# Performance work log

Hardware: AMD Instinct MI355X
Metric: run time of the kernel (lower is better)

## Reference

```python
import jax, jax.numpy as jnp
import numpy as np
import math

EMB, HEAD, B, S = 1024, 64, 4, 4096

def setup_inputs() -> dict:
    key = jax.random.key(0)
    ks = jax.random.split(key, 7)
    scale = 1.0 / math.sqrt(EMB)
    return {
        "x": jax.random.normal(ks[0], (B, S, EMB), dtype=jnp.float32),
        "Wq": jax.random.uniform(ks[1], (EMB, HEAD), jnp.float32, -scale, scale),
        "bq": jax.random.uniform(ks[2], (HEAD,), jnp.float32, -scale, scale),
        "Wk": jax.random.uniform(ks[3], (EMB, HEAD), jnp.float32, -scale, scale),
        "bk": jax.random.uniform(ks[4], (HEAD,), jnp.float32, -scale, scale),
        "Wv": jax.random.uniform(ks[5], (EMB, HEAD), jnp.float32, -scale, scale),
        "bv": jax.random.uniform(ks[6], (HEAD,), jnp.float32, -scale, scale),
    }

def reference(x, Wq, bq, Wk, bk, Wv, bv):
    # x: [B, S, E]
    q = x @ Wq + bq            # [B, S, H]
    k = x @ Wk + bk
    v = x @ Wv + bv
    scores = jnp.einsum('bqh,bkh->bqk', q, k) / math.sqrt(q.shape[-1])
    # causal mask: position q attends to k <= q
    s = x.shape[1]
    causal = jnp.tril(jnp.ones((s, s), dtype=bool))
    scores = jnp.where(causal, scores, -jnp.inf)
    attn = jax.nn.softmax(scores, axis=-1)
    return jnp.einsum('bqk,bkh->bqh', attn, v)
```

## Files before the change

### kernel.cpp

```cpp
#include <hip/hip_runtime.h>
#include <hip/hip_bf16.h>
#include <math.h>

#define EMB 1024
#define HEAD 64
#define NB 4
#define SEQ 4096
#define MTOT (NB * SEQ)
#define QSCALE (0.125f * 1.44269504088896f)
#define MBOUND 4.0f

typedef __attribute__((ext_vector_type(8))) short bf16x8;
typedef __attribute__((ext_vector_type(4))) float f32x4;
typedef __attribute__((ext_vector_type(16))) float f32x16;
typedef __attribute__((ext_vector_type(2))) unsigned u32x2;

static __device__ __forceinline__ unsigned short f2b(float f) {
    union { float f; unsigned u; } v; v.f = f;
    unsigned r = v.u + 0x7FFFu + ((v.u >> 16) & 1u);
    return (unsigned short)(r >> 16);
}
static __device__ __forceinline__ float b2f(unsigned short u) {
    union { unsigned u; float f; } v; v.u = ((unsigned)u) << 16; return v.f;
}
static __device__ __forceinline__ unsigned pk2(float lo, float hi) {
    unsigned r;
    asm("v_cvt_pk_bf16_f32 %0, %1, %2" : "=v"(r) : "v"(lo), "v"(hi));
    return r;
}
static __device__ __forceinline__ float ex2(float x) {
    float r;
    asm("v_exp_f32 %0, %1" : "=v"(r) : "v"(x));
    return r;
}

__global__ void wb_kernel(const float* __restrict__ Wq, const float* __restrict__ Wk,
                          const float* __restrict__ Wv, unsigned short* __restrict__ Wb) {
    const int f = blockIdx.x % 12, ks = blockIdx.x / 12;
    const int t = threadIdx.x;
    const int h = t >> 7, lane = (t >> 1) & 63, j0 = (t & 1) * 4;
    const int li = lane & 15, lg = lane >> 4;
    const float* W = (f < 4) ? Wq : (f < 8) ? Wk : Wv;
    const int nc = (f & 3) * 16 + li;
    const int k0 = ks * 64 + h * 32 + lg * 8 + j0;
    const unsigned u0 = pk2(W[(size_t)(k0 + 0) * HEAD + nc], W[(size_t)(k0 + 1) * HEAD + nc]);
    const unsigned u1 = pk2(W[(size_t)(k0 + 2) * HEAD + nc], W[(size_t)(k0 + 3) * HEAD + nc]);
    unsigned short* dst = Wb + (size_t)(f * 16 + ks) * 1024 + h * 512 + lane * 8 + j0;
    *(u32x2*)dst = (u32x2){u0, u1};
}

__global__ __launch_bounds__(256) void proj_kernel(
    const float* __restrict__ x, const unsigned short* __restrict__ Wb,
    const float* __restrict__ bq, const float* __restrict__ bk,
    const float* __restrict__ bv, unsigned short* __restrict__ qb,
    unsigned short* __restrict__ kb, unsigned short* __restrict__ vb) {
    __shared__ unsigned short Xl[16][1032];

    const int tid = threadIdx.x;
    const int nh = tid >> 6, lane = tid & 63;
    const int li = lane & 15, lg = lane >> 4;
    const int rbase = blockIdx.x * 16;

    {
        const int row = tid >> 4, cf = (tid & 15) * 8;
        const float* xr = x + (size_t)(rbase + row) * EMB;
#pragma unroll
        for (int j = 0; j < 8; ++j) {
            const int col = j * 128 + cf;
            const float4 t0 = *(const float4*)(xr + col);
            const float4 t1 = *(const float4*)(xr + col + 4);
            union { bf16x8 v; unsigned u[4]; } pa;
            pa.u[0] = pk2(t0.x, t0.y); pa.u[1] = pk2(t0.z, t0.w);
            pa.u[2] = pk2(t1.x, t1.y); pa.u[3] = pk2(t1.z, t1.w);
            *(bf16x8*)&Xl[row][col] = pa.v;
        }
    }
    __syncthreads();

    f32x4 acc[3];
#pragma unroll
    for (int n = 0; n < 3; ++n) acc[n] = (f32x4){0.f, 0.f, 0.f, 0.f};

    bf16x8 wreg[3][3][2];
#pragma unroll
    for (int p = 0; p < 2; ++p)
#pragma unroll
        for (int n = 0; n < 3; ++n) {
            const unsigned short* wp = Wb + (size_t)((nh * 3 + n) * 16 + p) * 1024 + lane * 8;
            wreg[p][n][0] = *(const bf16x8*)(wp);
            wreg[p][n][1] = *(const bf16x8*)(wp + 512);
        }
#pragma unroll
    for (int ks = 0; ks < 16; ++ks) {
        if (ks + 2 < 16) {
            const int slot = (ks + 2) % 3;
#pragma unroll
            for (int n = 0; n < 3; ++n) {
                const unsigned short* wp = Wb + (size_t)((nh * 3 + n) * 16 + ks + 2) * 1024 + lane * 8;
                wreg[slot][n][0] = *(const bf16x8*)(wp);
                wreg[slot][n][1] = *(const bf16x8*)(wp + 512);
            }
        }
        const int cur = ks % 3;
        const bf16x8 a0 = *(const bf16x8*)&Xl[li][ks * 64 + lg * 8];
        const bf16x8 a1 = *(const bf16x8*)&Xl[li][ks * 64 + 32 + lg * 8];
#pragma unroll
        for (int n = 0; n < 3; ++n) {
            const int f = nh * 3 + n;
            const bf16x8 b0 = wreg[cur][n][0];
            const bf16x8 b1 = wreg[cur][n][1];
            if (f < 8) {
                acc[n] = __builtin_amdgcn_mfma_f32_16x16x32_bf16(b0, a0, acc[n], 0, 0, 0);
                acc[n] = __builtin_amdgcn_mfma_f32_16x16x32_bf16(b1, a1, acc[n], 0, 0, 0);
            } else {
                acc[n] = __builtin_amdgcn_mfma_f32_16x16x32_bf16(a0, b0, acc[n], 0, 0, 0);
                acc[n] = __builtin_amdgcn_mfma_f32_16x16x32_bf16(a1, b1, acc[n], 0, 0, 0);
            }
        }
    }

    const int si0 = rbase & 4095, bi = rbase >> 12;
#pragma unroll
    for (int n = 0; n < 3; ++n) {
        const int f = nh * 3 + n;
        if (f < 8) {
            const float* bias = (f < 4) ? bq : bk;
            const int dbase = (f & 3) * 16 + lg * 4;
            const float4 bb = *(const float4*)&bias[dbase];
            const float qs = (f < 4) ? QSCALE : 1.0f;
            unsigned short* dst = (f < 4) ? qb : kb;
            const size_t plane = (size_t)((bi * 2 + (lg >> 1)) * 4 + (f & 3)) * (SEQ * 8);
            const unsigned u0 = pk2((acc[n][0] + bb.x) * qs, (acc[n][1] + bb.y) * qs);
            const unsigned u1 = pk2((acc[n][2] + bb.z) * qs, (acc[n][3] + bb.w) * qs);
            unsigned short* p = dst + plane + (size_t)(si0 + li) * 8 + (lg & 1) * 4;
            *(u32x2*)p = (u32x2){u0, u1};
        } else {
            const int nc = (f & 3) * 16 + li;
            const float bb = bv[nc];
            const unsigned u0 = pk2(acc[n][0] + bb, acc[n][1] + bb);
            const unsigned u1 = pk2(acc[n][2] + bb, acc[n][3] + bb);
            const int si = si0 + lg * 4;
            unsigned short* p = vb + ((size_t)bi * 512 + (si >> 3)) * 512 + nc * 8 + (si & 7);
            *(u32x2*)p = (u32x2){u0, u1};
        }
    }
}

template<int W64, int NWIN, int KMAX>
__global__ __launch_bounds__(64) void attn_kernel(
    const unsigned short* __restrict__ Qb, const unsigned short* __restrict__ Kb,
    const unsigned short* __restrict__ Vb, unsigned* __restrict__ pO,
    float* __restrict__ pL) {
    const int lane = threadIdx.x & 63;
    const int ql = lane & 31, h = lane >> 5;
    const int b = blockIdx.y;
    const int w = blockIdx.x;
    int seg = 0;
#pragma unroll
    for (int kk = 1; kk < KMAX; ++kk)
        if (w >= 128 * kk - W64 * kk * (kk - 1)) seg = kk;
    const int Os = 128 * seg - W64 * seg * (seg - 1);
    const int qidx = 2 * W64 * seg + (w - Os);
    const int tdiag = qidx >> 1;
    const int qa0 = qidx * 32;
    const int t0 = W64 * seg;
    const int tend = (t0 + W64 < tdiag + 1) ? t0 + W64 : tdiag + 1;

    const unsigned short* qb0 = Qb + ((size_t)(b * 2 + h)) * 4 * (SEQ * 8);
    const unsigned short* kb0 = Kb + ((size_t)(b * 2 + h)) * 4 * (SEQ * 8);
    const unsigned short* vb0 = Vb + (size_t)b * 512 * 512;

    bf16x8 qf[4];
#pragma unroll
    for (int s = 0; s < 4; ++s)
        qf[s] = *(const bf16x8*)(qb0 + (size_t)s * (SEQ * 8) + (size_t)(qa0 + ql) * 8);

    f32x16 oa0, oa1;
#pragma unroll
    for (int r = 0; r < 16; ++r) { oa0[r] = 0.f; oa1[r] = 0.f; }
    float lsum = 0.f;

    bf16x8 kcur[2][4], knxt[2][4];
#pragma unroll
    for (int hh = 0; hh < 2; ++hh)
#pragma unroll
        for (int s = 0; s < 4; ++s)
            kcur[hh][s] = *(const bf16x8*)(kb0 + (size_t)s * (SEQ * 8)
                                           + ((size_t)t0 * 64 + 32 * hh + ql) * 8);

    for (int t = t0; t < tend; ++t) {
        bf16x8 vf[2][4];
#pragma unroll
        for (int dt = 0; dt < 2; ++dt)
#pragma unroll
            for (int cc = 0; cc < 4; ++cc)
                vf[dt][cc] = *(const bf16x8*)(vb0 + ((size_t)t * 8 + 2 * cc + h) * 512
                                              + (dt * 32 + ql) * 8);
        if (t + 1 < tend) {
#pragma unroll
            for (int hh = 0; hh < 2; ++hh)
#pragma unroll
                for (int s = 0; s < 4; ++s)
                    knxt[hh][s] = *(const bf16x8*)(kb0 + (size_t)s * (SEQ * 8)
                                                   + ((size_t)(t + 1) * 64 + 32 * hh + ql) * 8);
        }

        f32x16 st0, st1;
#pragma unroll
        for (int r = 0; r < 16; ++r) { st0[r] = 0.f; st1[r] = 0.f; }
        __builtin_amdgcn_s_setprio(1);
#pragma unroll
        for (int s = 0; s < 4; ++s) {
            st0 = __builtin_amdgcn_mfma_f32_32x32x16_bf16(kcur[0][s], qf[s], st0, 0, 0, 0);
            st1 = __builtin_amdgcn_mfma_f32_32x32x16_bf16(kcur[1][s], qf[s], st1, 0, 0, 0);
        }
        __builtin_amdgcn_s_setprio(0);

        if (t == tdiag) {
            if (qidx & 1) {
#pragma unroll
                for (int r = 0; r < 16; ++r) {
                    const int kvl = (r & 3) + 8 * (r >> 2) + 4 * h;
                    if (kvl > ql) st1[r] = -1e30f;
                }
            } else {
#pragma unroll
                for (int r = 0; r < 16; ++r) {
                    const int kvl = (r & 3) + 8 * (r >> 2) + 4 * h;
                    if (kvl > ql) st0[r] = -1e30f;
                    st1[r] = -1e30f;
                }
            }
        }
#pragma unroll
        for (int r = 0; r < 16; ++r) {
            st0[r] = ex2(st0[r] - MBOUND);
            st1[r] = ex2(st1[r] - MBOUND);
        }
        {
            float q0 = (st0[0] + st0[1]) + (st0[2] + st0[3]);
            float q1 = (st0[4] + st0[5]) + (st0[6] + st0[7]);
            float q2 = (st0[8] + st0[9]) + (st0[10] + st0[11]);
            float q3 = (st0[12] + st0[13]) + (st0[14] + st0[15]);
            float q4 = (st1[0] + st1[1]) + (st1[2] + st1[3]);
            float q5 = (st1[4] + st1[5]) + (st1[6] + st1[7]);
            float q6 = (st1[8] + st1[9]) + (st1[10] + st1[11]);
            float q7 = (st1[12] + st1[13]) + (st1[14] + st1[15]);
            lsum += ((q0 + q1) + (q2 + q3)) + ((q4 + q5) + (q6 + q7));
        }

        bf16x8 bfv[4];
#pragma unroll
        for (int hh = 0; hh < 2; ++hh) {
            unsigned w8[8];
#pragma unroll
            for (int tt = 0; tt < 8; ++tt)
                w8[tt] = hh ? pk2(st1[2 * tt], st1[2 * tt + 1])
                            : pk2(st0[2 * tt], st0[2 * tt + 1]);
            const unsigned xa0 = h ? w8[0] : w8[2];
            const unsigned va0 = __shfl_xor((int)xa0, 32);
            const unsigned xb0 = h ? w8[1] : w8[3];
            const unsigned vb_0 = __shfl_xor((int)xb0, 32);
            union { bf16x8 v; unsigned u[4]; } bbv;
            bbv.u[0] = h ? va0 : w8[0];
            bbv.u[1] = h ? vb_0 : w8[1];
            bbv.u[2] = h ? w8[2] : va0;
            bbv.u[3] = h ? w8[3] : vb_0;
            bfv[hh * 2] = bbv.v;
            const unsigned xa1 = h ? w8[4] : w8[6];
            const unsigned va1 = __shfl_xor((int)xa1, 32);
            const unsigned xb1 = h ? w8[5] : w8[7];
            const unsigned vb_1 = __shfl_xor((int)xb1, 32);
            bbv.u[0] = h ? va1 : w8[4];
            bbv.u[1] = h ? vb_1 : w8[5];
            bbv.u[2] = h ? w8[6] : va1;
            bbv.u[3] = h ? w8[7] : vb_1;
            bfv[hh * 2 + 1] = bbv.v;
        }
        __builtin_amdgcn_s_setprio(1);
#pragma unroll
        for (int cc = 0; cc < 4; ++cc) {
            oa0 = __builtin_amdgcn_mfma_f32_32x32x16_bf16(vf[0][cc], bfv[cc], oa0, 0, 0, 0);
            oa1 = __builtin_amdgcn_mfma_f32_32x32x16_bf16(vf[1][cc], bfv[cc], oa1, 0, 0, 0);
        }
        __builtin_amdgcn_s_setprio(0);

#pragma unroll
        for (int hh = 0; hh < 2; ++hh)
#pragma unroll
            for (int s = 0; s < 4; ++s)
                kcur[hh][s] = knxt[hh][s];
    }

    lsum += __shfl_xor(lsum, 32);
    const size_t gw = (size_t)b * NWIN + w;
    unsigned* po = pO + gw * 1024;
#pragma unroll
    for (int r = 0; r < 16; r += 2) {
        const int dp = ((r & 3) >> 1) + 4 * (r >> 2) + 2 * h;
        po[dp * 32 + ql] = pk2(oa0[r], oa0[r + 1]);
        po[(16 + dp) * 32 + ql] = pk2(oa1[r], oa1[r + 1]);
    }
    if (h == 0) pL[gw * 32 + ql] = lsum;
}

template<int W64, int NWIN>
__global__ __launch_bounds__(256) void merge_kernel(
    const unsigned* __restrict__ pO, const float* __restrict__ pL,
    float* __restrict__ out) {
    const int qidx = blockIdx.x, b = blockIdx.y;
    const int wcount = qidx / (2 * W64) + 1;
    const int t = threadIdx.x;
    const int ql = t & 31, g = t >> 5;

    float acc[8] = {0.f, 0.f, 0.f, 0.f, 0.f, 0.f, 0.f, 0.f};
    float L = 0.f;
    for (int k = 0; k < wcount; ++k) {
        const int Os = 128 * k - W64 * k * (k - 1);
        const size_t gw = (size_t)b * NWIN + Os + (qidx - 2 * W64 * k);
        L += pL[gw * 32 + ql];
#pragma unroll
        for (int i = 0; i < 4; ++i) {
            const unsigned u = pO[gw * 1024 + (size_t)(g * 4 + i) * 32 + ql];
            acc[2 * i] += b2f((unsigned short)(u & 0xFFFFu));
            acc[2 * i + 1] += b2f((unsigned short)(u >> 16));
        }
    }
    const float inv = 1.0f / L;
    float* op = out + ((size_t)b * SEQ + qidx * 32 + ql) * HEAD + g * 8;
    f32x4 o0 = {acc[0] * inv, acc[1] * inv, acc[2] * inv, acc[3] * inv};
    f32x4 o1 = {acc[4] * inv, acc[5] * inv, acc[6] * inv, acc[7] * inv};
    *(f32x4*)(op) = o0;
    *(f32x4*)(op + 4) = o1;
}

extern "C" void kernel_launch(void* const* d_in, const int* in_sizes, int n_in,
                              void* d_out, int out_size, void* d_ws, size_t ws_size,
                              hipStream_t stream) {
    const float* x  = (const float*)d_in[0];
    const float* Wq = (const float*)d_in[1];
    const float* bq = (const float*)d_in[2];
    const float* Wk = (const float*)d_in[3];
    const float* bk = (const float*)d_in[4];
    const float* Wv = (const float*)d_in[5];
    const float* bv = (const float*)d_in[6];

    unsigned short* Wb = (unsigned short*)d_ws;
    unsigned short* qb = Wb + 3 * HEAD * EMB;
    unsigned short* kb = qb + (size_t)MTOT * HEAD;
    unsigned short* vb = kb + (size_t)MTOT * HEAD;
    unsigned* pO = (unsigned*)(vb + (size_t)MTOT * HEAD);
    const size_t base_shorts = (size_t)3 * HEAD * EMB + (size_t)3 * MTOT * HEAD;

    wb_kernel<<<dim3(192), dim3(256), 0, stream>>>(Wq, Wk, Wv, Wb);
    proj_kernel<<<dim3(MTOT / 16), dim3(256), 0, stream>>>(x, Wb, bq, bk, bv, qb, kb, vb);

    const size_t need8 = base_shorts * 2 + (size_t)NB * 576 * (1024 * 4 + 32 * 4);
    if (ws_size >= need8) {
        float* pL = (float*)(pO + (size_t)NB * 576 * 1024);
        attn_kernel<8, 576, 8><<<dim3(576, NB), dim3(64), 0, stream>>>(qb, kb, vb, pO, pL);
        merge_kernel<8, 576><<<dim3(128, NB), dim3(256), 0, stream>>>(pO, pL, (float*)d_out);
    } else {
        float* pL = (float*)(pO + (size_t)NB * 320 * 1024);
        attn_kernel<16, 320, 4><<<dim3(320, NB), dim3(64), 0, stream>>>(qb, kb, vb, pO, pL);
        merge_kernel<16, 320><<<dim3(128, NB), dim3(256), 0, stream>>>(pO, pL, (float*)d_out);
    }
}
```

Baseline: 62.12 us.

## Fuse split-KV merge into attention kernel via last-arriver atomic counter

Removes the separate merge kernel. Each attention workgroup now publishes its partial output, then increments a per-query-tile counter. The last workgroup to finish a tile reduces all partials and writes the normalized output. The counters are zeroed in the weight-conversion kernel, and the workspace-size fallback path is dropped. This saves a launch and its tail, at the cost of a serial reduction done by a single 64-thread wave per tile plus fence and atomic overhead.

After: 149.7 us. 141% more time.

```diff
diff --git a/kernel.cpp b/kernel.cpp
--- a/kernel.cpp
+++ b/kernel.cpp
@@ -35,7 +35,9 @@
 }
 
 __global__ void wb_kernel(const float* __restrict__ Wq, const float* __restrict__ Wk,
-                          const float* __restrict__ Wv, unsigned short* __restrict__ Wb) {
+                          const float* __restrict__ Wv, unsigned short* __restrict__ Wb,
+                          unsigned* __restrict__ cnt) {
+    if (blockIdx.x < 2) cnt[blockIdx.x * 256 + threadIdx.x] = 0;
     const int f = blockIdx.x % 12, ks = blockIdx.x / 12;
     const int t = threadIdx.x;
     const int h = t >> 7, lane = (t >> 1) & 63, j0 = (t & 1) * 4;
@@ -150,7 +152,7 @@
 __global__ __launch_bounds__(64) void attn_kernel(
     const unsigned short* __restrict__ Qb, const unsigned short* __restrict__ Kb,
     const unsigned short* __restrict__ Vb, unsigned* __restrict__ pO,
-    float* __restrict__ pL) {
+    float* __restrict__ pL, unsigned* __restrict__ cnt, float* __restrict__ out) {
     const int lane = threadIdx.x & 63;
     const int ql = lane & 31, h = lane >> 5;
     const int b = blockIdx.y;
@@ -302,36 +304,38 @@
         po[(16 + dp) * 32 + ql] = pk2(oa1[r], oa1[r + 1]);
     }
     if (h == 0) pL[gw * 32 + ql] = lsum;
-}
-
-template<int W64, int NWIN>
-__global__ __launch_bounds__(256) void merge_kernel(
-    const unsigned* __restrict__ pO, const float* __restrict__ pL,
-    float* __restrict__ out) {
-    const int qidx = blockIdx.x, b = blockIdx.y;
+
+    __threadfence();
+    int old = 0;
+    if (lane == 0) old = (int)atomicAdd(&cnt[b * 128 + qidx], 1u);
+    old = __shfl(old, 0);
     const int wcount = qidx / (2 * W64) + 1;
-    const int t = threadIdx.x;
-    const int ql = t & 31, g = t >> 5;
-
-    float acc[8] = {0.f, 0.f, 0.f, 0.f, 0.f, 0.f, 0.f, 0.f};
-    float L = 0.f;
-    for (int k = 0; k < wcount; ++k) {
-        const int Os = 128 * k - W64 * k * (k - 1);
-        const size_t gw = (size_t)b * NWIN + Os + (qidx - 2 * W64 * k);
-        L += pL[gw * 32 + ql];
-#pragma unroll
-        for (int i = 0; i < 4; ++i) {
-            const unsigned u = pO[gw * 1024 + (size_t)(g * 4 + i) * 32 + ql];
-            acc[2 * i] += b2f((unsigned short)(u & 0xFFFFu));
-            acc[2 * i + 1] += b2f((unsigned short)(u >> 16));
-        }
-    }
-    const float inv = 1.0f / L;
-    float* op = out + ((size_t)b * SEQ + qidx * 32 + ql) * HEAD + g * 8;
-    f32x4 o0 = {acc[0] * inv, acc[1] * inv, acc[2] * inv, acc[3] * inv};
-    f32x4 o1 = {acc[4] * inv, acc[5] * inv, acc[6] * inv, acc[7] * inv};
-    *(f32x4*)(op) = o0;
-    *(f32x4*)(op + 4) = o1;
+    if (old == wcount - 1) {
+        __threadfence();
+        float L = 0.f;
+        float acc[32];
+#pragma unroll
+        for (int i = 0; i < 32; ++i) acc[i] = 0.f;
+        for (int k = 0; k < wcount; ++k) {
+            const int Ok = 128 * k - W64 * k * (k - 1);
+            const size_t g2 = (size_t)b * NWIN + Ok + (qidx - 2 * W64 * k);
+            L += pL[g2 * 32 + ql];
+#pragma unroll
+            for (int i = 0; i < 16; ++i) {
+                const unsigned u = pO[g2 * 1024 + (size_t)(h * 16 + i) * 32 + ql];
+                acc[2 * i] += b2f((unsigned short)(u & 0xFFFFu));
+                acc[2 * i + 1] += b2f((unsigned short)(u >> 16));
+            }
+        }
+        const float inv = 1.0f / L;
+        float* op = out + ((size_t)b * SEQ + qidx * 32 + ql) * HEAD + h * 32;
+#pragma unroll
+        for (int i = 0; i < 8; ++i) {
+            f32x4 o = {acc[4 * i] * inv, acc[4 * i + 1] * inv,
+                       acc[4 * i + 2] * inv, acc[4 * i + 3] * inv};
+            *(f32x4*)(op + 4 * i) = o;
+        }
+    }
 }
 
 extern "C" void kernel_launch(void* const* d_in, const int* in_sizes, int n_in,
@@ -350,19 +354,11 @@
     unsigned short* kb = qb + (size_t)MTOT * HEAD;
     unsigned short* vb = kb + (size_t)MTOT * HEAD;
     unsigned* pO = (unsigned*)(vb + (size_t)MTOT * HEAD);
-    const size_t base_shorts = (size_t)3 * HEAD * EMB + (size_t)3 * MTOT * HEAD;
-
-    wb_kernel<<<dim3(192), dim3(256), 0, stream>>>(Wq, Wk, Wv, Wb);
+    float* pL = (float*)(pO + (size_t)NB * 576 * 1024);
+    unsigned* cnt = (unsigned*)(pL + (size_t)NB * 576 * 32);
+
+    wb_kernel<<<dim3(192), dim3(256), 0, stream>>>(Wq, Wk, Wv, Wb, cnt);
     proj_kernel<<<dim3(MTOT / 16), dim3(256), 0, stream>>>(x, Wb, bq, bk, bv, qb, kb, vb);
-
-    const size_t need8 = base_shorts * 2 + (size_t)NB * 576 * (1024 * 4 + 32 * 4);
-    if (ws_size >= need8) {
-        float* pL = (float*)(pO + (size_t)NB * 576 * 1024);
-        attn_kernel<8, 576, 8><<<dim3(576, NB), dim3(64), 0, stream>>>(qb, kb, vb, pO, pL);
-        merge_kernel<8, 576><<<dim3(128, NB), dim3(256), 0, stream>>>(pO, pL, (float*)d_out);
-    } else {
-        float* pL = (float*)(pO + (size_t)NB * 320 * 1024);
-        attn_kernel<16, 320, 4><<<dim3(320, NB), dim3(64), 0, stream>>>(qb, kb, vb, pO, pL);
-        merge_kernel<16, 320><<<dim3(128, NB), dim3(256), 0, stream>>>(pO, pL, (float*)d_out);
-    }
-}
+    attn_kernel<8, 576, 8><<<dim3(576, NB), dim3(64), 0, stream>>>(
+        qb, kb, vb, pO, pL, cnt, (float*)d_out);
+}
```
